# Kernel optimization log

Hardware: AMD Instinct MI355X
Metric: run time of the kernel (lower is better)

The kernel has to match this reference:

```python
import jax, jax.numpy as jnp
import numpy as np

IMG = 224
PATCH_SIZE = 2      # stride of the output patch grid (output_size = H // PATCH_SIZE)
PATCH_PIXEL = 4     # samples per patch side (deformable resampling resolution)
EMBED = 192
OFFSET_EMBED = 2    # (dx, dy) per patch
IN_CH = 3
BATCH = 32


def setup_inputs() -> dict:
    key = jax.random.key(0)
    k1, k2, k3 = jax.random.split(key, 3)
    x = jax.random.normal(k1, (BATCH, IN_CH, IMG, IMG), jnp.float32)
    conv_w = jax.random.normal(k2, (EMBED, IN_CH, 3, 3), jnp.float32) * 0.05
    conv_b = jnp.zeros((EMBED,), jnp.float32)
    off_w = jax.random.normal(k3, (OFFSET_EMBED, EMBED), jnp.float32) * 0.02
    return {"x": x, "conv_w": conv_w, "conv_b": conv_b, "off_w": off_w}


def _bilinear_gather(img, ys, xs):
    # img: [B, C, H, W]; ys, xs: [B, P] float pixel coords. Border-clamped bilinear.
    B, C, H, W = img.shape
    y0 = jnp.floor(ys)
    x0 = jnp.floor(xs)
    wy = (ys - y0)[:, None, :]
    wx = (xs - x0)[:, None, :]
    y0i = jnp.clip(y0.astype(jnp.int32), 0, H - 1)
    y1i = jnp.clip(y0i + 1, 0, H - 1)
    x0i = jnp.clip(x0.astype(jnp.int32), 0, W - 1)
    x1i = jnp.clip(x0i + 1, 0, W - 1)
    flat = img.reshape(B, C, H * W)
    P = ys.shape[1]

    def g(yi, xi):
        idx = (yi * W + xi)[:, None, :]  # [B,1,P]
        return jnp.take_along_axis(flat, jnp.broadcast_to(idx, (B, C, P)), axis=2)

    v00 = g(y0i, x0i)
    v01 = g(y0i, x1i)
    v10 = g(y1i, x0i)
    v11 = g(y1i, x1i)
    return (v00 * (1 - wy) * (1 - wx) + v01 * (1 - wy) * wx
            + v10 * wy * (1 - wx) + v11 * wy * wx)  # [B,C,P]


def reference(x, conv_w, conv_b, off_w):
    B, C, H, W = x.shape
    # PatchEmbed: conv k3 s2 p1 -> flatten -> tokens [B, N, E]
    feat = jax.lax.conv_general_dilated(
        x, conv_w, window_strides=(2, 2), padding=((1, 1), (1, 1)),
        dimension_numbers=('NCHW', 'OIHW', 'NCHW')) + conv_b[None, :, None, None]
    Hf, Wf = feat.shape[2], feat.shape[3]
    tokens = feat.reshape(B, EMBED, Hf * Wf).transpose(0, 2, 1)  # [B,N,E]
    # offset predictor: GELU (exact) then bias-free linear
    pred = jax.nn.gelu(tokens, approximate=False) @ off_w.T      # [B,N,2]

    Ho, Wo = H // PATCH_SIZE, W // PATCH_SIZE  # == (Hf, Wf) by construction
    off = pred.reshape(B, Ho, Wo, OFFSET_EMBED) * PATCH_SIZE     # pixel-space offsets

    # Deformable patch resampling: each output patch samples a PATCH_PIXEL^2 grid
    # centered at its shifted patch center.
    cy = (jnp.arange(Ho, dtype=jnp.float32) + 0.5) * PATCH_SIZE
    cx = (jnp.arange(Wo, dtype=jnp.float32) + 0.5) * PATCH_SIZE
    local = ((jnp.arange(PATCH_PIXEL, dtype=jnp.float32) + 0.5) / PATCH_PIXEL
             * PATCH_SIZE - PATCH_SIZE / 2)
    ys = (cy[None, :, None, None, None] + off[..., 1][:, :, :, None, None]
          + local[None, None, None, :, None])
    xs = (cx[None, None, :, None, None] + off[..., 0][:, :, :, None, None]
          + local[None, None, None, None, :])
    shape5 = (B, Ho, Wo, PATCH_PIXEL, PATCH_PIXEL)
    ys = jnp.broadcast_to(ys, shape5).reshape(B, -1)
    xs = jnp.broadcast_to(xs, shape5).reshape(B, -1)

    sampled = _bilinear_gather(x, ys, xs)  # [B,C,Ho*Wo*pp*pp]
    out = sampled.reshape(B, C, Ho, Wo, PATCH_PIXEL, PATCH_PIXEL)
    out = out.transpose(0, 1, 2, 4, 3, 5).reshape(
        B, C, Ho * PATCH_PIXEL, Wo * PATCH_PIXEL)
    return out
```

## Files before the change

kernel.cpp:

```cpp
#include <hip/hip_runtime.h>

#define IMG   224
#define IMG2  (IMG * IMG)
#define HO    112
#define WO_   112
#define EMBED 192
#define BATCH 32
#define NPOS  (BATCH * HO * WO_)
#define PPB   (HO * WO_)
#define BLK_POS 128
#define TPW   4

typedef __attribute__((ext_vector_type(8))) short short8;
typedef __attribute__((ext_vector_type(4))) float float4v;

__device__ __forceinline__ short f2bf(float f) {
    unsigned u = __builtin_bit_cast(unsigned, f);
    u += 0x7FFFu + ((u >> 16) & 1u);
    return (short)(u >> 16);
}

__device__ __forceinline__ float fast_gelu(float a) {
    float e = __builtin_amdgcn_exp2f(a * -2.45546507f);
    return a * __builtin_amdgcn_rcpf(1.0f + e);
}

__global__ __launch_bounds__(128)
void fused_kernel(const float* __restrict__ x,
                  const float* __restrict__ conv_w,
                  const float* __restrict__ conv_b,
                  const float* __restrict__ off_w,
                  float* __restrict__ out) {
    const int lane = threadIdx.x & 63;
    const int wv   = threadIdx.x >> 6;
    const int col  = lane & 15;
    const int quad = lane >> 4;

    const int b   = blockIdx.x / (PPB / BLK_POS);
    const int pb0 = (blockIdx.x % (PPB / BLK_POS)) * BLK_POS + wv * 64;
    const float* __restrict__ xb = x + (size_t)b * 3 * IMG2;
    float* __restrict__ ob = out + (size_t)b * 3 * (448 * 448);

    int  off[8];
    bool isr[8];
    bool k27[8];
#pragma unroll
    for (int j = 0; j < 8; ++j) {
        int k = quad * 8 + j;
        int c = k / 9, r9 = k % 9;
        int dy = r9 / 3, dx = r9 % 3;
        isr[j] = (k < 27);
        k27[j] = (k == 27);
        off[j] = isr[j] ? (c * IMG2 + dy * IMG + dx) : 0;
    }

    short8 bfrag[12];
#pragma unroll
    for (int nt = 0; nt < 12; ++nt) {
        int ch = nt * 16 + col;
#pragma unroll
        for (int j = 0; j < 8; ++j) {
            int k = quad * 8 + j;
            float v = (k < 27) ? conv_w[ch * 27 + k]
                               : ((k == 27) ? conv_b[ch] : 0.0f);
            bfrag[nt][j] = f2bf(v);
        }
    }
    float owx[12], owy[12];
#pragma unroll
    for (int nt = 0; nt < 12; ++nt) {
        owx[nt] = off_w[nt * 16 + col] * 2.0f;
        owy[nt] = off_w[EMBED + nt * 16 + col] * 2.0f;
    }

    for (int it = 0; it < TPW; ++it) {
        int p   = pb0 + it * 16;
        int ho  = p / WO_;
        int wo0 = p % WO_;
        int iy0 = 2 * ho - 1;
        int ixl = 2 * (wo0 + col) - 1;
        int base = iy0 * IMG + ixl;

        short8 a;
        if (ho > 0 && wo0 > 0) {
#pragma unroll
            for (int j = 0; j < 8; ++j) {
                float v = isr[j] ? xb[base + off[j]] : 0.0f;
                if (k27[j]) v = 1.0f;
                a[j] = f2bf(v);
            }
        } else {
#pragma unroll
            for (int j = 0; j < 8; ++j) {
                int k = quad * 8 + j;
                int r9 = k % 9;
                int dy = r9 / 3, dx = r9 % 3;
                bool ok = isr[j] && (iy0 + dy >= 0) && (ixl + dx >= 0);
                int ad = ok ? (base + off[j]) : 0;
                float v = ok ? xb[ad] : 0.0f;
                if (k27[j]) v = 1.0f;
                a[j] = f2bf(v);
            }
        }

        float ox[4] = {0, 0, 0, 0}, oy[4] = {0, 0, 0, 0};
#pragma unroll
        for (int nt = 0; nt < 12; ++nt) {
            float4v c = {0.0f, 0.0f, 0.0f, 0.0f};
            c = __builtin_amdgcn_mfma_f32_16x16x32_bf16(a, bfrag[nt], c, 0, 0, 0);
#pragma unroll
            for (int r = 0; r < 4; ++r) {
                float g = fast_gelu(c[r]);
                ox[r] = fmaf(g, owx[nt], ox[r]);
                oy[r] = fmaf(g, owy[nt], oy[r]);
            }
        }
#pragma unroll
        for (int d = 1; d < 16; d <<= 1) {
#pragma unroll
            for (int r = 0; r < 4; ++r) {
                ox[r] += __shfl_xor(ox[r], d, 64);
                oy[r] += __shfl_xor(oy[r], d, 64);
            }
        }

        int patch = lane >> 2;
        int rsel  = patch & 3;
        int px    = lane & 3;
        float s01x = (rsel & 1) ? ox[1] : ox[0];
        float s23x = (rsel & 1) ? ox[3] : ox[2];
        float ofx  = (rsel & 2) ? s23x : s01x;
        float s01y = (rsel & 1) ? oy[1] : oy[0];
        float s23y = (rsel & 1) ? oy[3] : oy[2];
        float ofy  = (rsel & 2) ? s23y : s01y;

        int wo = wo0 + patch;
        float xs = 2.0f * wo + 0.25f + 0.5f * px + ofx;
        float x0f = floorf(xs);
        float wx  = xs - x0f;
        int x0 = (int)x0f; x0 = min(max(x0, 0), IMG - 1);
        int xq = min(x0, IMG - 2);
        bool selx = (x0 > xq);
        int ocol = wo * 4 + px;

#pragma unroll
        for (int py = 0; py < 4; ++py) {
            float ys = 2.0f * ho + 0.25f + 0.5f * py + ofy;
            float y0f = floorf(ys);
            float wy  = ys - y0f;
            int y0 = (int)y0f; y0 = min(max(y0, 0), IMG - 1);
            int dyo = (y0 < IMG - 1) ? IMG : 0;
            int rb = y0 * IMG + xq;
            int orow = (ho * 4 + py) * 448 + ocol;

#pragma unroll
            for (int c = 0; c < 3; ++c) {
                int v0 = rb + c * IMG2;
                int v1 = v0 + dyo;
                float A0 = xb[v0], A1 = xb[v0 + 1];
                float B0 = xb[v1], B1 = xb[v1 + 1];
                float v00 = selx ? A1 : A0;
                float v10 = selx ? B1 : B0;
                float top = fmaf(wx, A1 - v00, v00);
                float bot = fmaf(wx, B1 - v10, v10);
                ob[c * 200704 + orow] = fmaf(wy, bot - top, top);
            }
        }
    }
}

extern "C" void kernel_launch(void* const* d_in, const int* in_sizes, int n_in,
                              void* d_out, int out_size, void* d_ws, size_t ws_size,
                              hipStream_t stream) {
    const float* x      = (const float*)d_in[0];
    const float* conv_w = (const float*)d_in[1];
    const float* conv_b = (const float*)d_in[2];
    const float* off_w  = (const float*)d_in[3];
    float* out = (float*)d_out;

    fused_kernel<<<NPOS / BLK_POS, 128, 0, stream>>>(x, conv_w, conv_b, off_w, out);
}
```

Measured before the change: 153.5 us.

## Split fused kernel into offset-prediction and resampling kernels via workspace

The single fused kernel is split in two. The first kernel computes per-patch offsets with MFMA and writes them to a workspace buffer. The second kernel resamples with 256-thread blocks and a higher occupancy bound. This decouples the register-heavy MFMA stage from the memory-bound gather/store stage so each can run at its own occupancy, at the cost of an extra launch and a small round-trip through global memory. The original fused path stays as a fallback when no workspace is available.

```diff
diff --git a/kernel.cpp b/kernel.cpp
--- a/kernel.cpp
+++ b/kernel.cpp
@@ -6,13 +6,12 @@
 #define WO_   112
 #define EMBED 192
 #define BATCH 32
-#define NPOS  (BATCH * HO * WO_)
 #define PPB   (HO * WO_)
-#define BLK_POS 128
-#define TPW   4
+#define NPOS  (BATCH * PPB)
 
 typedef __attribute__((ext_vector_type(8))) short short8;
 typedef __attribute__((ext_vector_type(4))) float float4v;
+typedef __attribute__((ext_vector_type(2))) float float2v;
 
 __device__ __forceinline__ short f2bf(float f) {
     unsigned u = __builtin_bit_cast(unsigned, f);
@@ -23,6 +22,192 @@
 __device__ __forceinline__ float fast_gelu(float a) {
     float e = __builtin_amdgcn_exp2f(a * -2.45546507f);
     return a * __builtin_amdgcn_rcpf(1.0f + e);
+}
+
+__device__ __forceinline__ void tile_offsets(
+    const float* __restrict__ xb,
+    const short8* __restrict__ bfrag,
+    const float* __restrict__ owx, const float* __restrict__ owy,
+    const int* __restrict__ offj, const bool* __restrict__ isr,
+    const bool* __restrict__ k27,
+    int ho, int wo0, int col, int quad,
+    float ox[4], float oy[4])
+{
+    int iy0 = 2 * ho - 1;
+    int ixl = 2 * (wo0 + col) - 1;
+    int base = iy0 * IMG + ixl;
+
+    short8 a;
+    if (ho > 0 && wo0 > 0) {
+#pragma unroll
+        for (int j = 0; j < 8; ++j) {
+            float v = isr[j] ? xb[base + offj[j]] : 0.0f;
+            if (k27[j]) v = 1.0f;
+            a[j] = f2bf(v);
+        }
+    } else {
+#pragma unroll
+        for (int j = 0; j < 8; ++j) {
+            int k  = quad * 8 + j;
+            int r9 = k % 9;
+            int dy = r9 / 3, dx = r9 % 3;
+            bool ok = isr[j] && (iy0 + dy >= 0) && (ixl + dx >= 0);
+            int ad = ok ? (base + offj[j]) : 0;
+            float v = ok ? xb[ad] : 0.0f;
+            if (k27[j]) v = 1.0f;
+            a[j] = f2bf(v);
+        }
+    }
+
+    ox[0] = ox[1] = ox[2] = ox[3] = 0.0f;
+    oy[0] = oy[1] = oy[2] = oy[3] = 0.0f;
+#pragma unroll
+    for (int nt = 0; nt < 12; ++nt) {
+        float4v c = {0.0f, 0.0f, 0.0f, 0.0f};
+        c = __builtin_amdgcn_mfma_f32_16x16x32_bf16(a, bfrag[nt], c, 0, 0, 0);
+#pragma unroll
+        for (int r = 0; r < 4; ++r) {
+            float g = fast_gelu(c[r]);
+            ox[r] = fmaf(g, owx[nt], ox[r]);
+            oy[r] = fmaf(g, owy[nt], oy[r]);
+        }
+    }
+#pragma unroll
+    for (int d = 1; d < 16; d <<= 1) {
+#pragma unroll
+        for (int r = 0; r < 4; ++r) {
+            ox[r] += __shfl_xor(ox[r], d, 64);
+            oy[r] += __shfl_xor(oy[r], d, 64);
+        }
+    }
+}
+
+__device__ __forceinline__ void resample_patch(
+    const float* __restrict__ xb, float* __restrict__ ob,
+    int ho, int wo, int px, float ofx, float ofy)
+{
+    float xs  = 2.0f * wo + 0.25f + 0.5f * px + ofx;
+    float x0f = floorf(xs);
+    float wx  = xs - x0f;
+    int x0 = (int)x0f; x0 = min(max(x0, 0), IMG - 1);
+    int xq = min(x0, IMG - 2);
+    bool selx = (x0 > xq);
+    int ocol = wo * 4 + px;
+
+#pragma unroll
+    for (int py = 0; py < 4; ++py) {
+        float ys  = 2.0f * ho + 0.25f + 0.5f * py + ofy;
+        float y0f = floorf(ys);
+        float wy  = ys - y0f;
+        int y0 = (int)y0f; y0 = min(max(y0, 0), IMG - 1);
+        int dyo = (y0 < IMG - 1) ? IMG : 0;
+        int rb = y0 * IMG + xq;
+        int orow = (ho * 4 + py) * 448 + ocol;
+
+#pragma unroll
+        for (int c = 0; c < 3; ++c) {
+            int v0 = rb + c * IMG2;
+            int v1 = v0 + dyo;
+            float A0 = xb[v0], A1 = xb[v0 + 1];
+            float B0 = xb[v1], B1 = xb[v1 + 1];
+            float v00 = selx ? A1 : A0;
+            float v10 = selx ? B1 : B0;
+            float top = fmaf(wx, A1 - v00, v00);
+            float bot = fmaf(wx, B1 - v10, v10);
+            ob[c * 200704 + orow] = fmaf(wy, bot - top, top);
+        }
+    }
+}
+
+__global__ __launch_bounds__(128)
+void offsets_kernel(const float* __restrict__ x,
+                    const float* __restrict__ conv_w,
+                    const float* __restrict__ conv_b,
+                    const float* __restrict__ off_w,
+                    float2v* __restrict__ offs) {
+    const int lane = threadIdx.x & 63;
+    const int wv   = threadIdx.x >> 6;
+    const int col  = lane & 15;
+    const int quad = lane >> 4;
+
+    const int b   = blockIdx.x / (PPB / 128);
+    const int pb0 = (blockIdx.x % (PPB / 128)) * 128 + wv * 64;
+    const float* __restrict__ xb = x + (size_t)b * 3 * IMG2;
+
+    int  offj[8];
+    bool isr[8], k27[8];
+#pragma unroll
+    for (int j = 0; j < 8; ++j) {
+        int k = quad * 8 + j;
+        int c = k / 9, r9 = k % 9;
+        int dy = r9 / 3, dx = r9 % 3;
+        isr[j] = (k < 27);
+        k27[j] = (k == 27);
+        offj[j] = isr[j] ? (c * IMG2 + dy * IMG + dx) : 0;
+    }
+
+    short8 bfrag[12];
+#pragma unroll
+    for (int nt = 0; nt < 12; ++nt) {
+        int ch = nt * 16 + col;
+#pragma unroll
+        for (int j = 0; j < 8; ++j) {
+            int k = quad * 8 + j;
+            float v = (k < 27) ? conv_w[ch * 27 + k]
+                               : ((k == 27) ? conv_b[ch] : 0.0f);
+            bfrag[nt][j] = f2bf(v);
+        }
+    }
+    float owx[12], owy[12];
+#pragma unroll
+    for (int nt = 0; nt < 12; ++nt) {
+        owx[nt] = off_w[nt * 16 + col] * 2.0f;
+        owy[nt] = off_w[EMBED + nt * 16 + col] * 2.0f;
+    }
+
+    for (int it = 0; it < 4; ++it) {
+        int p   = pb0 + it * 16;
+        int ho  = p / WO_;
+        int wo0 = p % WO_;
+
+        float ox[4], oy[4];
+        tile_offsets(xb, bfrag, owx, owy, offj, isr, k27,
+                     ho, wo0, col, quad, ox, oy);
+
+        int rsel = col & 3;
+        float sx01 = (rsel & 1) ? ox[1] : ox[0];
+        float sx23 = (rsel & 1) ? ox[3] : ox[2];
+        float vx   = (rsel & 2) ? sx23 : sx01;
+        float sy01 = (rsel & 1) ? oy[1] : oy[0];
+        float sy23 = (rsel & 1) ? oy[3] : oy[2];
+        float vy   = (rsel & 2) ? sy23 : sy01;
+        if (col < 4) {
+            int gpos = blockIdx.x * 128 + wv * 64 + it * 16 + quad * 4 + rsel;
+            float2v o; o[0] = vx; o[1] = vy;
+            offs[gpos] = o;
+        }
+    }
+}
+
+__global__ __launch_bounds__(256, 8)
+void resample_kernel(const float* __restrict__ x,
+                     const float2v* __restrict__ offs,
+                     float* __restrict__ out) {
+    const int lane  = threadIdx.x & 63;
+    const int wv    = threadIdx.x >> 6;
+    const int patch = lane >> 2;
+    const int px    = lane & 3;
+
+    const int b  = blockIdx.x / (PPB / 64);
+    const int sb = (blockIdx.x % (PPB / 64)) * 64 + wv * 16;
+    const int ho  = sb / WO_;
+    const int wo0 = sb % WO_;
+
+    const float* __restrict__ xb = x + (size_t)b * 3 * IMG2;
+    float* __restrict__ ob = out + (size_t)b * 3 * (448 * 448);
+
+    float2v o = offs[blockIdx.x * 64 + wv * 16 + patch];
+    resample_patch(xb, ob, ho, wo0 + patch, px, o[0], o[1]);
 }
 
 __global__ __launch_bounds__(128)
@@ -36,14 +221,13 @@
     const int col  = lane & 15;
     const int quad = lane >> 4;
 
-    const int b   = blockIdx.x / (PPB / BLK_POS);
-    const int pb0 = (blockIdx.x % (PPB / BLK_POS)) * BLK_POS + wv * 64;
+    const int b   = blockIdx.x / (PPB / 128);
+    const int pb0 = (blockIdx.x % (PPB / 128)) * 128 + wv * 64;
     const float* __restrict__ xb = x + (size_t)b * 3 * IMG2;
     float* __restrict__ ob = out + (size_t)b * 3 * (448 * 448);
 
-    int  off[8];
-    bool isr[8];
-    bool k27[8];
+    int  offj[8];
+    bool isr[8], k27[8];
 #pragma unroll
     for (int j = 0; j < 8; ++j) {
         int k = quad * 8 + j;
@@ -51,9 +235,8 @@
         int dy = r9 / 3, dx = r9 % 3;
         isr[j] = (k < 27);
         k27[j] = (k == 27);
-        off[j] = isr[j] ? (c * IMG2 + dy * IMG + dx) : 0;
-    }
-
+        offj[j] = isr[j] ? (c * IMG2 + dy * IMG + dx) : 0;
+    }
     short8 bfrag[12];
 #pragma unroll
     for (int nt = 0; nt < 12; ++nt) {
@@ -73,99 +256,26 @@
         owy[nt] = off_w[EMBED + nt * 16 + col] * 2.0f;
     }
 
-    for (int it = 0; it < TPW; ++it) {
+    for (int it = 0; it < 4; ++it) {
         int p   = pb0 + it * 16;
         int ho  = p / WO_;
         int wo0 = p % WO_;
-        int iy0 = 2 * ho - 1;
-        int ixl = 2 * (wo0 + col) - 1;
-        int base = iy0 * IMG + ixl;
-
-        short8 a;
-        if (ho > 0 && wo0 > 0) {
-#pragma unroll
-            for (int j = 0; j < 8; ++j) {
-                float v = isr[j] ? xb[base + off[j]] : 0.0f;
-                if (k27[j]) v = 1.0f;
-                a[j] = f2bf(v);
-            }
-        } else {
-#pragma unroll
-            for (int j = 0; j < 8; ++j) {
-                int k = quad * 8 + j;
-                int r9 = k % 9;
-                int dy = r9 / 3, dx = r9 % 3;
-                bool ok = isr[j] && (iy0 + dy >= 0) && (ixl + dx >= 0);
-                int ad = ok ? (base + off[j]) : 0;
-                float v = ok ? xb[ad] : 0.0f;
-                if (k27[j]) v = 1.0f;
-                a[j] = f2bf(v);
-            }
-        }
-
-        float ox[4] = {0, 0, 0, 0}, oy[4] = {0, 0, 0, 0};
-#pragma unroll
-        for (int nt = 0; nt < 12; ++nt) {
-            float4v c = {0.0f, 0.0f, 0.0f, 0.0f};
-            c = __builtin_amdgcn_mfma_f32_16x16x32_bf16(a, bfrag[nt], c, 0, 0, 0);
-#pragma unroll
-            for (int r = 0; r < 4; ++r) {
-                float g = fast_gelu(c[r]);
-                ox[r] = fmaf(g, owx[nt], ox[r]);
-                oy[r] = fmaf(g, owy[nt], oy[r]);
-            }
-        }
-#pragma unroll
-        for (int d = 1; d < 16; d <<= 1) {
-#pragma unroll
-            for (int r = 0; r < 4; ++r) {
-                ox[r] += __shfl_xor(ox[r], d, 64);
-                oy[r] += __shfl_xor(oy[r], d, 64);
-            }
-        }
+
+        float ox[4], oy[4];
+        tile_offsets(xb, bfrag, owx, owy, offj, isr, k27,
+                     ho, wo0, col, quad, ox, oy);
 
         int patch = lane >> 2;
         int rsel  = patch & 3;
         int px    = lane & 3;
-        float s01x = (rsel & 1) ? ox[1] : ox[0];
-        float s23x = (rsel & 1) ? ox[3] : ox[2];
-        float ofx  = (rsel & 2) ? s23x : s01x;
-        float s01y = (rsel & 1) ? oy[1] : oy[0];
-        float s23y = (rsel & 1) ? oy[3] : oy[2];
-        float ofy  = (rsel & 2) ? s23y : s01y;
-
-        int wo = wo0 + patch;
-        float xs = 2.0f * wo + 0.25f + 0.5f * px + ofx;
-        float x0f = floorf(xs);
-        float wx  = xs - x0f;
-        int x0 = (int)x0f; x0 = min(max(x0, 0), IMG - 1);
-        int xq = min(x0, IMG - 2);
-        bool selx = (x0 > xq);
-        int ocol = wo * 4 + px;
-
-#pragma unroll
-        for (int py = 0; py < 4; ++py) {
-            float ys = 2.0f * ho + 0.25f + 0.5f * py + ofy;
-            float y0f = floorf(ys);
-            float wy  = ys - y0f;
-            int y0 = (int)y0f; y0 = min(max(y0, 0), IMG - 1);
-            int dyo = (y0 < IMG - 1) ? IMG : 0;
-            int rb = y0 * IMG + xq;
-            int orow = (ho * 4 + py) * 448 + ocol;
-
-#pragma unroll
-            for (int c = 0; c < 3; ++c) {
-                int v0 = rb + c * IMG2;
-                int v1 = v0 + dyo;
-                float A0 = xb[v0], A1 = xb[v0 + 1];
-                float B0 = xb[v1], B1 = xb[v1 + 1];
-                float v00 = selx ? A1 : A0;
-                float v10 = selx ? B1 : B0;
-                float top = fmaf(wx, A1 - v00, v00);
-                float bot = fmaf(wx, B1 - v10, v10);
-                ob[c * 200704 + orow] = fmaf(wy, bot - top, top);
-            }
-        }
+        float sx01 = (rsel & 1) ? ox[1] : ox[0];
+        float sx23 = (rsel & 1) ? ox[3] : ox[2];
+        float ofx  = (rsel & 2) ? sx23 : sx01;
+        float sy01 = (rsel & 1) ? oy[1] : oy[0];
+        float sy23 = (rsel & 1) ? oy[3] : oy[2];
+        float ofy  = (rsel & 2) ? sy23 : sy01;
+
+        resample_patch(xb, ob, ho, wo0 + patch, px, ofx, ofy);
     }
 }
 
@@ -178,5 +288,12 @@
     const float* off_w  = (const float*)d_in[3];
     float* out = (float*)d_out;
 
-    fused_kernel<<<NPOS / BLK_POS, 128, 0, stream>>>(x, conv_w, conv_b, off_w, out);
-}
+    const size_t need = (size_t)NPOS * sizeof(float2v);
+    if (d_ws != nullptr && ws_size >= need) {
+        float2v* offs = (float2v*)d_ws;
+        offsets_kernel<<<NPOS / 128, 128, 0, stream>>>(x, conv_w, conv_b, off_w, offs);
+        resample_kernel<<<NPOS / 64, 256, 0, stream>>>(x, offs, out);
+    } else {
+        fused_kernel<<<NPOS / 128, 128, 0, stream>>>(x, conv_w, conv_b, off_w, out);
+    }
+}
```

New measurement: 154.8 us. About the same (+0.8%).

## Split work across more waves, polynomial GELU, packed bf16 converts and vector loads

Applied to the files above, without the earlier changes.

Each block now has 4 waves, each handling 2 tiles of 16 positions instead of 4 sequential tiles per wave, with both tiles gathered and run through MFMA before resampling. This gives more waves per CU and more independent work to overlap latency. GELU becomes a clamped polynomial approximation instead of exp+rcp, and bf16 conversion uses v_cvt_pk_bf16_f32. Weight loads and the bilinear pair loads are vectorised. The polynomial GELU may change the predicted offsets slightly, and the 8-byte pair loads may not be 8-byte aligned.

```diff
diff --git a/kernel.cpp b/kernel.cpp
--- a/kernel.cpp
+++ b/kernel.cpp
@@ -6,44 +6,158 @@
 #define WO_   112
 #define EMBED 192
 #define BATCH 32
-#define NPOS  (BATCH * HO * WO_)
 #define PPB   (HO * WO_)
-#define BLK_POS 128
-#define TPW   4
+#define NPOS  (BATCH * PPB)
 
 typedef __attribute__((ext_vector_type(8))) short short8;
 typedef __attribute__((ext_vector_type(4))) float float4v;
-
-__device__ __forceinline__ short f2bf(float f) {
-    unsigned u = __builtin_bit_cast(unsigned, f);
-    u += 0x7FFFu + ((u >> 16) & 1u);
-    return (short)(u >> 16);
+typedef __attribute__((ext_vector_type(2))) float float2v;
+typedef __attribute__((ext_vector_type(4))) unsigned uint4v;
+
+__device__ __forceinline__ unsigned cvt_pk_bf16(float lo, float hi) {
+    unsigned r;
+    asm("v_cvt_pk_bf16_f32 %0, %1, %2" : "=v"(r) : "v"(lo), "v"(hi));
+    return r;
+}
+
+__device__ __forceinline__ float2v load2(const float* __restrict__ p) {
+    float2v r;
+    __builtin_memcpy(&r, p, 8);
+    return r;
+}
+__device__ __forceinline__ float4v load4(const float* __restrict__ p) {
+    float4v r;
+    __builtin_memcpy(&r, p, 16);
+    return r;
 }
 
 __device__ __forceinline__ float fast_gelu(float a) {
-    float e = __builtin_amdgcn_exp2f(a * -2.45546507f);
-    return a * __builtin_amdgcn_rcpf(1.0f + e);
-}
-
-__global__ __launch_bounds__(128)
-void fused_kernel(const float* __restrict__ x,
-                  const float* __restrict__ conv_w,
-                  const float* __restrict__ conv_b,
-                  const float* __restrict__ off_w,
-                  float* __restrict__ out) {
+    float t = a * a;
+    float p = fmaf(t, fmaf(t, fmaf(t, -0.0035665f, 0.0255793f),
+                           -0.1018611f), 0.4255f);
+    float q = fmaf(a, p, 0.5f);
+    q = fminf(fmaxf(q, 0.0f), 1.0f);
+    return a * q;
+}
+
+__device__ __forceinline__ void resample_patch(
+    const float* __restrict__ xb, float* __restrict__ ob,
+    int ho, int wo, int px, float ofx, float ofy)
+{
+    float xs  = 2.0f * wo + 0.25f + 0.5f * px + ofx;
+    float x0f = floorf(xs);
+    float wx  = xs - x0f;
+    int x0 = (int)x0f; x0 = min(max(x0, 0), IMG - 1);
+    int xq = min(x0, IMG - 2);
+    bool selx = (x0 > xq);
+    int ocol = wo * 4 + px;
+
+#pragma unroll
+    for (int py = 0; py < 4; ++py) {
+        float ys  = 2.0f * ho + 0.25f + 0.5f * py + ofy;
+        float y0f = floorf(ys);
+        float wy  = ys - y0f;
+        int y0 = (int)y0f; y0 = min(max(y0, 0), IMG - 1);
+        int dyo = (y0 < IMG - 1) ? IMG : 0;
+        int rb = y0 * IMG + xq;
+        int orow = (ho * 4 + py) * 448 + ocol;
+
+#pragma unroll
+        for (int c = 0; c < 3; ++c) {
+            int v0 = rb + c * IMG2;
+            float2v A = load2(xb + v0);
+            float2v B = load2(xb + v0 + dyo);
+            float v00 = selx ? A[1] : A[0];
+            float v10 = selx ? B[1] : B[0];
+            float top = fmaf(wx, A[1] - v00, v00);
+            float bot = fmaf(wx, B[1] - v10, v10);
+            ob[c * 200704 + orow] = fmaf(wy, bot - top, top);
+        }
+    }
+}
+
+__device__ __forceinline__ short8 gather_tile(
+    const float* __restrict__ xb, int ho, int wo0, int col, int quad,
+    const int* __restrict__ offj, const bool* __restrict__ isr,
+    const bool* __restrict__ k27)
+{
+    int iy0 = 2 * ho - 1;
+    int ixl = 2 * (wo0 + col) - 1;
+    int base = iy0 * IMG + ixl;
+    float v[8];
+    if (ho > 0 && wo0 > 0) {
+#pragma unroll
+        for (int j = 0; j < 8; ++j) {
+            float t = isr[j] ? xb[base + offj[j]] : 0.0f;
+            v[j] = k27[j] ? 1.0f : t;
+        }
+    } else {
+#pragma unroll
+        for (int j = 0; j < 8; ++j) {
+            int k  = quad * 8 + j;
+            int r9 = k % 9;
+            int dy = r9 / 3, dx = r9 % 3;
+            bool ok = isr[j] && (iy0 + dy >= 0) && (ixl + dx >= 0);
+            int ad = ok ? (base + offj[j]) : 0;
+            float t = ok ? xb[ad] : 0.0f;
+            v[j] = k27[j] ? 1.0f : t;
+        }
+    }
+    uint4v au = {cvt_pk_bf16(v[0], v[1]), cvt_pk_bf16(v[2], v[3]),
+                 cvt_pk_bf16(v[4], v[5]), cvt_pk_bf16(v[6], v[7])};
+    return __builtin_bit_cast(short8, au);
+}
+
+__device__ __forceinline__ float2v tile_offsets(
+    short8 a, const short8* __restrict__ bfrag,
+    const float2v* __restrict__ owp, int lane)
+{
+    float2v acc[4];
+#pragma unroll
+    for (int r = 0; r < 4; ++r) acc[r] = (float2v){0.0f, 0.0f};
+#pragma unroll
+    for (int nt = 0; nt < 12; ++nt) {
+        float4v c = {0.0f, 0.0f, 0.0f, 0.0f};
+        c = __builtin_amdgcn_mfma_f32_16x16x32_bf16(a, bfrag[nt], c, 0, 0, 0);
+#pragma unroll
+        for (int r = 0; r < 4; ++r) {
+            float g = fast_gelu(c[r]);
+            acc[r] += owp[nt] * g;
+        }
+    }
+#pragma unroll
+    for (int d = 1; d < 16; d <<= 1) {
+#pragma unroll
+        for (int r = 0; r < 4; ++r) {
+            acc[r][0] += __shfl_xor(acc[r][0], d, 64);
+            acc[r][1] += __shfl_xor(acc[r][1], d, 64);
+        }
+    }
+    int rsel = (lane >> 2) & 3;
+    float2v s01 = (rsel & 1) ? acc[1] : acc[0];
+    float2v s23 = (rsel & 1) ? acc[3] : acc[2];
+    return (rsel & 2) ? s23 : s01;
+}
+
+__global__ __launch_bounds__(256)
+void fused2_kernel(const float* __restrict__ x,
+                   const float* __restrict__ conv_w,
+                   const float* __restrict__ conv_b,
+                   const float* __restrict__ off_w,
+                   float* __restrict__ out) {
     const int lane = threadIdx.x & 63;
     const int wv   = threadIdx.x >> 6;
     const int col  = lane & 15;
     const int quad = lane >> 4;
 
-    const int b   = blockIdx.x / (PPB / BLK_POS);
-    const int pb0 = (blockIdx.x % (PPB / BLK_POS)) * BLK_POS + wv * 64;
+    const int b  = blockIdx.x / (PPB / 128);
+    const int p0 = (blockIdx.x % (PPB / 128)) * 128 + wv * 32;
+    const int p1 = p0 + 16;
     const float* __restrict__ xb = x + (size_t)b * 3 * IMG2;
     float* __restrict__ ob = out + (size_t)b * 3 * (448 * 448);
 
-    int  off[8];
-    bool isr[8];
-    bool k27[8];
+    int  offj[8];
+    bool isr[8], k27[8];
 #pragma unroll
     for (int j = 0; j < 8; ++j) {
         int k = quad * 8 + j;
@@ -51,122 +165,51 @@
         int dy = r9 / 3, dx = r9 % 3;
         isr[j] = (k < 27);
         k27[j] = (k == 27);
-        off[j] = isr[j] ? (c * IMG2 + dy * IMG + dx) : 0;
+        offj[j] = isr[j] ? (c * IMG2 + dy * IMG + dx) : 0;
     }
 
     short8 bfrag[12];
 #pragma unroll
     for (int nt = 0; nt < 12; ++nt) {
         int ch = nt * 16 + col;
-#pragma unroll
-        for (int j = 0; j < 8; ++j) {
-            int k = quad * 8 + j;
-            float v = (k < 27) ? conv_w[ch * 27 + k]
-                               : ((k == 27) ? conv_b[ch] : 0.0f);
-            bfrag[nt][j] = f2bf(v);
-        }
-    }
-    float owx[12], owy[12];
+        const float* w = conv_w + ch * 27 + quad * 8;
+        float v[8];
+        if (quad < 3) {
+            float4v lo = load4(w);
+            float4v hi = load4(w + 4);
+            v[0] = lo[0]; v[1] = lo[1]; v[2] = lo[2]; v[3] = lo[3];
+            v[4] = hi[0]; v[5] = hi[1]; v[6] = hi[2]; v[7] = hi[3];
+        } else {
+            float2v lo = load2(w);
+            v[0] = lo[0]; v[1] = lo[1]; v[2] = w[2];
+            v[3] = conv_b[ch];
+            v[4] = v[5] = v[6] = v[7] = 0.0f;
+        }
+        uint4v pu = {cvt_pk_bf16(v[0], v[1]), cvt_pk_bf16(v[2], v[3]),
+                     cvt_pk_bf16(v[4], v[5]), cvt_pk_bf16(v[6], v[7])};
+        bfrag[nt] = __builtin_bit_cast(short8, pu);
+    }
+
+    float2v owp[12];
 #pragma unroll
     for (int nt = 0; nt < 12; ++nt) {
-        owx[nt] = off_w[nt * 16 + col] * 2.0f;
-        owy[nt] = off_w[EMBED + nt * 16 + col] * 2.0f;
-    }
-
-    for (int it = 0; it < TPW; ++it) {
-        int p   = pb0 + it * 16;
-        int ho  = p / WO_;
-        int wo0 = p % WO_;
-        int iy0 = 2 * ho - 1;
-        int ixl = 2 * (wo0 + col) - 1;
-        int base = iy0 * IMG + ixl;
-
-        short8 a;
-        if (ho > 0 && wo0 > 0) {
-#pragma unroll
-            for (int j = 0; j < 8; ++j) {
-                float v = isr[j] ? xb[base + off[j]] : 0.0f;
-                if (k27[j]) v = 1.0f;
-                a[j] = f2bf(v);
-            }
-        } else {
-#pragma unroll
-            for (int j = 0; j < 8; ++j) {
-                int k = quad * 8 + j;
-                int r9 = k % 9;
-                int dy = r9 / 3, dx = r9 % 3;
-                bool ok = isr[j] && (iy0 + dy >= 0) && (ixl + dx >= 0);
-                int ad = ok ? (base + off[j]) : 0;
-                float v = ok ? xb[ad] : 0.0f;
-                if (k27[j]) v = 1.0f;
-                a[j] = f2bf(v);
-            }
-        }
-
-        float ox[4] = {0, 0, 0, 0}, oy[4] = {0, 0, 0, 0};
-#pragma unroll
-        for (int nt = 0; nt < 12; ++nt) {
-            float4v c = {0.0f, 0.0f, 0.0f, 0.0f};
-            c = __builtin_amdgcn_mfma_f32_16x16x32_bf16(a, bfrag[nt], c, 0, 0, 0);
-#pragma unroll
-            for (int r = 0; r < 4; ++r) {
-                float g = fast_gelu(c[r]);
-                ox[r] = fmaf(g, owx[nt], ox[r]);
-                oy[r] = fmaf(g, owy[nt], oy[r]);
-            }
-        }
-#pragma unroll
-        for (int d = 1; d < 16; d <<= 1) {
-#pragma unroll
-            for (int r = 0; r < 4; ++r) {
-                ox[r] += __shfl_xor(ox[r], d, 64);
-                oy[r] += __shfl_xor(oy[r], d, 64);
-            }
-        }
-
-        int patch = lane >> 2;
-        int rsel  = patch & 3;
-        int px    = lane & 3;
-        float s01x = (rsel & 1) ? ox[1] : ox[0];
-        float s23x = (rsel & 1) ? ox[3] : ox[2];
-        float ofx  = (rsel & 2) ? s23x : s01x;
-        float s01y = (rsel & 1) ? oy[1] : oy[0];
-        float s23y = (rsel & 1) ? oy[3] : oy[2];
-        float ofy  = (rsel & 2) ? s23y : s01y;
-
-        int wo = wo0 + patch;
-        float xs = 2.0f * wo + 0.25f + 0.5f * px + ofx;
-        float x0f = floorf(xs);
-        float wx  = xs - x0f;
-        int x0 = (int)x0f; x0 = min(max(x0, 0), IMG - 1);
-        int xq = min(x0, IMG - 2);
-        bool selx = (x0 > xq);
-        int ocol = wo * 4 + px;
-
-#pragma unroll
-        for (int py = 0; py < 4; ++py) {
-            float ys = 2.0f * ho + 0.25f + 0.5f * py + ofy;
-            float y0f = floorf(ys);
-            float wy  = ys - y0f;
-            int y0 = (int)y0f; y0 = min(max(y0, 0), IMG - 1);
-            int dyo = (y0 < IMG - 1) ? IMG : 0;
-            int rb = y0 * IMG + xq;
-            int orow = (ho * 4 + py) * 448 + ocol;
-
-#pragma unroll
-            for (int c = 0; c < 3; ++c) {
-                int v0 = rb + c * IMG2;
-                int v1 = v0 + dyo;
-                float A0 = xb[v0], A1 = xb[v0 + 1];
-                float B0 = xb[v1], B1 = xb[v1 + 1];
-                float v00 = selx ? A1 : A0;
-                float v10 = selx ? B1 : B0;
-                float top = fmaf(wx, A1 - v00, v00);
-                float bot = fmaf(wx, B1 - v10, v10);
-                ob[c * 200704 + orow] = fmaf(wy, bot - top, top);
-            }
-        }
-    }
+        owp[nt] = (float2v){ off_w[nt * 16 + col] * 2.0f,
+                             off_w[EMBED + nt * 16 + col] * 2.0f };
+    }
+
+    const int ho0 = p0 / WO_, wo00 = p0 % WO_;
+    const int ho1 = p1 / WO_, wo01 = p1 % WO_;
+
+    short8 a0 = gather_tile(xb, ho0, wo00, col, quad, offj, isr, k27);
+    short8 a1 = gather_tile(xb, ho1, wo01, col, quad, offj, isr, k27);
+
+    float2v of0 = tile_offsets(a0, bfrag, owp, lane);
+    float2v of1 = tile_offsets(a1, bfrag, owp, lane);
+
+    int patch = lane >> 2;
+    int px    = lane & 3;
+    resample_patch(xb, ob, ho0, wo00 + patch, px, of0[0], of0[1]);
+    resample_patch(xb, ob, ho1, wo01 + patch, px, of1[0], of1[1]);
 }
 
 extern "C" void kernel_launch(void* const* d_in, const int* in_sizes, int n_in,
@@ -178,5 +221,5 @@
     const float* off_w  = (const float*)d_in[3];
     float* out = (float*)d_out;
 
-    fused_kernel<<<NPOS / BLK_POS, 128, 0, stream>>>(x, conv_w, conv_b, off_w, out);
-}
+    fused2_kernel<<<NPOS / 128, 256, 0, stream>>>(x, conv_w, conv_b, off_w, out);
+}
```

Measured after the change: 141.9 us. 7.6% less time.
